# Kernel tuning notes

Measured on AMD Instinct MI355X. Metric: run time of the kernel, lower is better.

The kernel has to match this reference:

```python
import jax, jax.numpy as jnp
from jax import lax
import numpy as np

# Lorentz manifold parameter (geoopt convention: hyperboloid <x,x>_L = -K, x0 = sqrt(K + ||x_s||^2)).
# curvature=1.0, learn_curvature=False in the selected config.
K = 1.0
SK = 1.0  # sqrt(K)
EPS = 1e-5


def l_inner(u, v):
    # Minkowski inner product with keepdim: -u0*v0 + <u_space, v_space>
    uv = u * v
    return -uv[..., :1] + jnp.sum(uv[..., 1:], axis=-1, keepdims=True)


def add_time(space):
    # CustomLorentz.add_time / calc_time: recompute time component from space part
    t = jnp.sqrt(jnp.sum(space * space, axis=-1, keepdims=True) + K)
    return jnp.concatenate([t, space], axis=-1)


def centroid(x):
    # Lorentz centroid over axis=-2 (CustomLorentz.centroid)
    avg = jnp.mean(x, axis=-2)
    den = jnp.sqrt(jnp.clip(jnp.abs(-l_inner(avg, avg)), 1e-8))
    return SK * avg / den


def lorentz_bn(x, beta, gamma):
    # LorentzBatchNorm (training mode, batch statistics). x: (B, N, C)
    mean = centroid(centroid(x))  # (C,) double centroid for 3D input
    # logmap(mean, x)
    xy = l_inner(mean, x)  # (B,N,1)
    dist = SK * jnp.arccosh(jnp.clip(-xy / K, 1.0 + 1e-7))
    nomin = x + (xy / K) * mean
    den = jnp.sqrt(jnp.clip(l_inner(nomin, nomin), 1e-8))
    u = dist * nomin / den
    # transp0back(mean, u): parallel transport mean -> origin
    o = jnp.zeros_like(mean).at[0].set(SK)
    u = u + (-SK * u[..., :1]) / (K + SK * mean[0]) * (mean + o)
    # Frechet variance (mean tangent norm) and rescale
    var = jnp.mean(jnp.linalg.norm(u, axis=-1))
    u = u * (gamma / (var + EPS))
    # transp0(beta, u): origin -> beta, then expmap at beta
    ob = jnp.zeros_like(beta).at[0].set(SK)
    u = u + l_inner(beta, u) / (K + SK * beta[0]) * (ob + beta)
    nu = jnp.sqrt(jnp.clip(l_inner(u, u), 1e-8))
    return jnp.cosh(nu / SK) * beta + SK * jnp.sinh(nu / SK) * u / nu


def lorentz_conv_block(x, W, b, beta, gamma):
    # LConv2d_Block: LorentzConv2d(3x3, stride 2, pad 1) + LorentzBatchNorm2d + relu-on-space
    B = x.shape[0]
    KK = 9  # kernel_size**2
    p = lax.conv_general_dilated_patches(
        jnp.transpose(x, (0, 3, 1, 2)), (3, 3), (2, 2), ((1, 1), (1, 1)))
    p = jnp.transpose(p, (0, 2, 3, 1))  # (B,Ho,Wo,C*9), channel-major = torch.nn.Unfold layout
    # Lorentz direct concatenation of the 9 patch points: fix zero padding, rescale time
    t = jnp.maximum(p[..., :KK], SK)
    t_new = jnp.sqrt(jnp.sum(t * t, axis=-1, keepdims=True) - (KK - 1) * K)
    pre = jnp.concatenate([t_new, p[..., KK:]], axis=-1)
    # LorentzFullyConnected: linear, drop produced time column, recompute time
    lin = jnp.einsum('bhwi,oi->bhwo', pre, W) + b
    y = add_time(lin[..., 1:])
    Ho, Wo, C = y.shape[1], y.shape[2], y.shape[3]
    y = lorentz_bn(y.reshape(B, Ho * Wo, C), beta, gamma).reshape(B, Ho, Wo, C)
    return add_time(jax.nn.relu(y[..., 1:]))


def setup_inputs() -> dict:
    key = jax.random.key(0)
    ks = jax.random.split(key, 12)
    B = 32
    inp = {"x": jax.random.normal(ks[0], (B, 3, 256, 256), jnp.float32)}
    # (out_channels, (in_channels-1)*9+1) per LorentzConv2d linearized kernel
    dims = [(33, 28), (65, 289), (129, 577), (257, 1153)]
    for i, (o, ii) in enumerate(dims):
        inp[f"conv_w{i}"] = 0.02 * jax.random.normal(ks[1 + i], (o, ii), jnp.float32)
        inp[f"conv_b{i}"] = jnp.zeros((o,), jnp.float32)
        inp[f"bn_beta{i}"] = jnp.zeros((o,), jnp.float32).at[0].set(SK)  # manifold origin
        inp[f"bn_gamma{i}"] = jnp.ones((1,), jnp.float32)
    flat = 16 * 16 * 256  # z_h*z_w*z_filters
    inp["wm"] = 0.02 * jax.random.normal(ks[8], (513, flat + 1), jnp.float32)
    inp["bm"] = jnp.zeros((513,), jnp.float32)
    inp["wv"] = 0.02 * jax.random.normal(ks[9], (513, flat + 1), jnp.float32)
    inp["bv"] = jnp.zeros((513,), jnp.float32)
    return inp


def reference(x, conv_w0, conv_b0, bn_beta0, bn_gamma0,
              conv_w1, conv_b1, bn_beta1, bn_gamma1,
              conv_w2, conv_b2, bn_beta2, bn_gamma2,
              conv_w3, conv_b3, bn_beta3, bn_gamma3,
              wm, bm, wv, bv):
    h = jnp.transpose(x, (0, 2, 3, 1))  # (B,H,W,3)
    # F.pad with zero time then manifold.projx == recompute time from space
    h = add_time(h)
    for W, b, beta, g in ((conv_w0, conv_b0, bn_beta0, bn_gamma0),
                          (conv_w1, conv_b1, bn_beta1, bn_gamma1),
                          (conv_w2, conv_b2, bn_beta2, bn_gamma2),
                          (conv_w3, conv_b3, bn_beta3, bn_gamma3)):
        h = lorentz_conv_block(h, W, b, beta, g)
    # lorentz_flatten: concat space parts, recompute single time
    h = add_time(h[..., 1:].reshape(h.shape[0], -1))  # (B, 65537)
    mean = add_time((h @ wm.T + bm)[..., 1:])          # (B, 513)
    varl = add_time((h @ wv.T + bv)[..., 1:])
    var = jnp.maximum(jax.nn.softplus(varl[..., 1:]), EPS)  # (B, 512)
    return mean, var
```

## Files before the change

kernel.cpp:

```cpp
#include <hip/hip_runtime.h>
#include <math.h>

#define DEV __device__ __forceinline__

typedef float f32x4 __attribute__((ext_vector_type(4)));
typedef __bf16 bf16x8 __attribute__((ext_vector_type(8)));

DEV unsigned short f2bf(float f){
  unsigned int u = __float_as_uint(f);
  u = (u + 0x7FFFu + ((u >> 16) & 1u)) >> 16;
  return (unsigned short)u;
}
DEV float bf2f(unsigned short s){
  return __uint_as_float(((unsigned int)s) << 16);
}

DEV float wredf(float v){
  v += __shfl_xor(v, 32, 64);
  v += __shfl_xor(v, 16, 64);
  v += __shfl_xor(v, 8, 64);
  v += __shfl_xor(v, 4, 64);
  v += __shfl_xor(v, 2, 64);
  v += __shfl_xor(v, 1, 64);
  return v;
}

__global__ void h0_kernel(const float* __restrict__ x, unsigned short* __restrict__ h0){
  int idx = blockIdx.x*256 + threadIdx.x;
  int b = idx >> 16, p = idx & 65535;
  const float* xb = x + (size_t)b*3*65536;
  float v0 = xb[p], v1 = xb[65536 + p], v2 = xb[131072 + p];
  float t = sqrtf(v0*v0 + v1*v1 + v2*v2 + 1.f);
  ushort4 o;
  o.x = f2bf(t); o.y = f2bf(v0); o.z = f2bf(v1); o.w = f2bf(v2);
  *(ushort4*)&h0[(size_t)idx*4] = o;
}

__global__ void wrepack_kernel(const float* __restrict__ w, unsigned short* __restrict__ dst,
                               int coutm1, int cs, int K, int krow){
  int idx = blockIdx.x*256 + threadIdx.x;
  if (idx >= coutm1*krow) return;
  int n = idx / krow, kk = idx - n*krow;
  unsigned short v = 0;
  if (kk < 9*cs){
    int kp = kk / cs, c = kk - kp*cs;
    v = f2bf(w[(size_t)(n+1)*K + 1 + c*9 + kp]);
  }
  dst[idx] = v;
}

__global__ __launch_bounds__(256) void conv0_mfma_kernel(
    const unsigned short* __restrict__ h0bf, const unsigned short* __restrict__ wrp0,
    const float* __restrict__ Wm, const float* __restrict__ bias,
    float* __restrict__ y, float* __restrict__ red){
  __shared__ __align__(16) unsigned short A_lds[64][40];
  __shared__ __align__(16) unsigned short B_lds[32][40];
  __shared__ float Tsq[64][9];
  __shared__ float tA[64];
  __shared__ float bins[33];
  int tid = threadIdx.x;
  int tile = blockIdx.x, b = blockIdx.y;
  int oy0 = (tile >> 4) * 8, ox0 = (tile & 15) * 8;
  for (int i = tid; i < 320; i += 256){
    uint4 z = {0,0,0,0};
    *(uint4*)&A_lds[i/5][(i%5)*8] = z;
  }
  if (tid < 128)
    *(uint4*)&B_lds[tid>>2][(tid&3)*8] = *(const uint4*)&wrp0[(size_t)(tid>>2)*32 + (tid&3)*8];
  if (tid < 33) bins[tid] = 0.f;
  __syncthreads();
  for (int i = tid; i < 576; i += 256){
    int m = i/9, kp = i - (i/9)*9;
    int py = oy0 + (m >> 3), px = ox0 + (m & 7);
    int iy = py*2 + kp/3 - 1, ix = px*2 + kp%3 - 1;
    ushort4 v = {0x3F80, 0, 0, 0};
    if ((unsigned)iy < 256u && (unsigned)ix < 256u)
      v = *(const ushort4*)&h0bf[((size_t)(b*256 + iy)*256 + ix)*4];
    A_lds[m][kp*3 + 0] = v.y;
    A_lds[m][kp*3 + 1] = v.z;
    A_lds[m][kp*3 + 2] = v.w;
    float tv = fmaxf(bf2f(v.x), 1.f);
    Tsq[m][kp] = tv*tv;
  }
  __syncthreads();
  if (tid < 64){
    float s = 0.f;
    #pragma unroll
    for (int kp = 0; kp < 9; ++kp) s += Tsq[tid][kp];
    tA[tid] = sqrtf(fmaxf(s - 8.f, 0.f));
  }
  int wave = tid >> 6, lane = tid & 63;
  int row = lane & 15, kb = lane >> 4;
  int m0 = wave * 16;
  f32x4 zero = {0.f,0.f,0.f,0.f};
  f32x4 acc0 = zero, acc1 = zero;
  bf16x8 af = *(const bf16x8*)&A_lds[m0 + row][kb*8];
  bf16x8 b0 = *(const bf16x8*)&B_lds[row][kb*8];
  bf16x8 b1 = *(const bf16x8*)&B_lds[16 + row][kb*8];
  acc0 = __builtin_amdgcn_mfma_f32_16x16x32_bf16(af, b0, acc0, 0, 0, 0);
  acc1 = __builtin_amdgcn_mfma_f32_16x16x32_bf16(af, b1, acc1, 0, 0, 0);
  __syncthreads();
  int o0 = row + 1, o1 = 17 + row;
  float bv0 = bias[o0], w00 = Wm[(size_t)o0*28];
  float bv1 = bias[o1], w01 = Wm[(size_t)o1*28];
  float v0[4], v1[4];
  #pragma unroll
  for (int r = 0; r < 4; ++r){
    int m = m0 + kb*4 + r;
    v0[r] = acc0[r] + bv0 + tA[m]*w00;
    v1[r] = acc1[r] + bv1 + tA[m]*w01;
    int py = oy0 + (m >> 3), px = ox0 + (m & 7);
    size_t pb_ = ((size_t)(b*128 + py)*128 + px)*33;
    y[pb_ + o0] = v0[r];
    y[pb_ + o1] = v1[r];
  }
  float sq[4];
  #pragma unroll
  for (int r = 0; r < 4; ++r) sq[r] = v0[r]*v0[r] + v1[r]*v1[r];
  #pragma unroll
  for (int msk = 1; msk <= 8; msk <<= 1)
    #pragma unroll
    for (int r = 0; r < 4; ++r) sq[r] += __shfl_xor(sq[r], msk, 64);
  float tvs = 0.f;
  #pragma unroll
  for (int r = 0; r < 4; ++r){
    float tv = sqrtf(sq[r] + 1.f);
    tvs += tv;
    if (row == 0){
      int m = m0 + kb*4 + r;
      int py = oy0 + (m >> 3), px = ox0 + (m & 7);
      y[((size_t)(b*128 + py)*128 + px)*33] = tv;
    }
  }
  float cs0 = v0[0] + v0[1] + v0[2] + v0[3];
  float cs1 = v1[0] + v1[1] + v1[2] + v1[3];
  cs0 += __shfl_xor(cs0, 16, 64); cs0 += __shfl_xor(cs0, 32, 64);
  cs1 += __shfl_xor(cs1, 16, 64); cs1 += __shfl_xor(cs1, 32, 64);
  tvs += __shfl_xor(tvs, 16, 64); tvs += __shfl_xor(tvs, 32, 64);
  if (kb == 0){
    atomicAdd(&bins[o0], cs0);
    atomicAdd(&bins[o1], cs1);
    if (row == 0) atomicAdd(&bins[0], tvs);
  }
  __syncthreads();
  if (tid < 33) atomicAdd(&red[(size_t)b*33 + tid], bins[tid]);
}

template<int CS, int COUT, int KPC, int NSPLIT, bool FUSE>
__global__ __launch_bounds__(256) void conv2_mfma_kernel(
    const unsigned short* __restrict__ sp_in, const unsigned short* __restrict__ t_in,
    const unsigned short* __restrict__ wrp, const float* __restrict__ Wm,
    const float* __restrict__ bias, float* __restrict__ y,
    float* __restrict__ red, int Hin, int Ho){
  constexpr int KROW = 9*CS;
  __shared__ __align__(16) unsigned short A_lds[64][40];
  __shared__ __align__(16) unsigned short B_lds[64][40];
  __shared__ float tA[64];
  __shared__ float ssqS[FUSE ? 64 : 1];
  __shared__ float binsS[FUSE ? COUT : 1];
  int tid = threadIdx.x;
  int wave = tid >> 6, lane = tid & 63;
  int tilesX = Ho >> 3;
  int tile = blockIdx.x, b = blockIdx.y;
  int zt = blockIdx.z / NSPLIT, sp = blockIdx.z % NSPLIT;
  int zbase = zt * 64;
  int oy0 = (tile / tilesX) * 8, ox0 = (tile % tilesX) * 8;
  int m0 = (wave >> 1) * 32, n0 = (wave & 1) * 32;
  int row = lane & 15, kb = lane >> 4;
  if (FUSE){
    if (tid < 64) ssqS[tid] = 0.f;
    for (int i = tid; i < COUT; i += 256) binsS[i] = 0.f;
  }
  if (sp == 0 && tid < 64){
    int m = tid;
    int py = oy0 + (m >> 3), px = ox0 + (m & 7);
    float s = 0.f;
    #pragma unroll
    for (int kp = 0; kp < 9; ++kp){
      int iy = py*2 + kp/3 - 1, ix = px*2 + kp%3 - 1;
      float tv = 1.f;
      if ((unsigned)iy < (unsigned)Hin && (unsigned)ix < (unsigned)Hin)
        tv = fmaxf(bf2f(t_in[(size_t)(b*Hin + iy)*Hin + ix]), 1.f);
      s = fmaf(tv, tv, s);
    }
    tA[m] = sqrtf(fmaxf(s - 8.f, 0.f));
  }
  f32x4 zero = {0.f,0.f,0.f,0.f};
  f32x4 acc[2][2] = {{zero,zero},{zero,zero}};
  int ar = tid >> 2, aseg = tid & 3;
  int apy = oy0 + (ar >> 3), apx = ox0 + (ar & 7);
  for (int ch = sp*KPC; ch < sp*KPC + KPC; ++ch){
    int kglob = ch * 32;
    int kp = kglob / CS, c0 = kglob % CS;
    int iy = apy*2 + kp/3 - 1, ix = apx*2 + kp%3 - 1;
    uint4 va = {0,0,0,0};
    if ((unsigned)iy < (unsigned)Hin && (unsigned)ix < (unsigned)Hin)
      va = *(const uint4*)&sp_in[((size_t)(b*Hin + iy)*Hin + ix)*CS + c0 + aseg*8];
    uint4 vb = *(const uint4*)&wrp[(size_t)(zbase + ar)*KROW + kglob + aseg*8];
    __syncthreads();
    *(uint4*)&A_lds[ar][aseg*8] = va;
    *(uint4*)&B_lds[ar][aseg*8] = vb;
    __syncthreads();
    bf16x8 af0 = *(const bf16x8*)&A_lds[m0 + row][kb*8];
    bf16x8 af1 = *(const bf16x8*)&A_lds[m0 + 16 + row][kb*8];
    bf16x8 bf0 = *(const bf16x8*)&B_lds[n0 + row][kb*8];
    bf16x8 bf1 = *(const bf16x8*)&B_lds[n0 + 16 + row][kb*8];
    acc[0][0] = __builtin_amdgcn_mfma_f32_16x16x32_bf16(af0, bf0, acc[0][0], 0, 0, 0);
    acc[0][1] = __builtin_amdgcn_mfma_f32_16x16x32_bf16(af0, bf1, acc[0][1], 0, 0, 0);
    acc[1][0] = __builtin_amdgcn_mfma_f32_16x16x32_bf16(af1, bf0, acc[1][0], 0, 0, 0);
    acc[1][1] = __builtin_amdgcn_mfma_f32_16x16x32_bf16(af1, bf1, acc[1][1], 0, 0, 0);
  }
  __syncthreads();
  float vv[2][2][4];
  #pragma unroll
  for (int mi = 0; mi < 2; ++mi)
    #pragma unroll
    for (int ni = 0; ni < 2; ++ni){
      int col = n0 + 16*ni + row;
      int o = zbase + 1 + col;
      float bv = 0.f, w0 = 0.f;
      if (sp == 0){ bv = bias[o]; w0 = Wm[(size_t)o*(KROW + 1)]; }
      #pragma unroll
      for (int r = 0; r < 4; ++r){
        int m = m0 + 16*mi + kb*4 + r;
        int py = oy0 + (m >> 3), px = ox0 + (m & 7);
        size_t idx = ((size_t)(b*Ho + py)*Ho + px)*COUT + o;
        float val = acc[mi][ni][r];
        if (sp == 0) val += bv + tA[m]*w0;
        vv[mi][ni][r] = val;
        if (NSPLIT > 1) atomicAdd(&y[idx], val);
        else            y[idx] = val;
      }
    }
  if (FUSE){
    float sq[2][4];
    #pragma unroll
    for (int mi = 0; mi < 2; ++mi)
      #pragma unroll
      for (int r = 0; r < 4; ++r)
        sq[mi][r] = vv[mi][0][r]*vv[mi][0][r] + vv[mi][1][r]*vv[mi][1][r];
    #pragma unroll
    for (int msk = 1; msk <= 8; msk <<= 1)
      #pragma unroll
      for (int mi = 0; mi < 2; ++mi)
        #pragma unroll
        for (int r = 0; r < 4; ++r) sq[mi][r] += __shfl_xor(sq[mi][r], msk, 64);
    if (row == 0){
      #pragma unroll
      for (int mi = 0; mi < 2; ++mi)
        #pragma unroll
        for (int r = 0; r < 4; ++r)
          atomicAdd(&ssqS[m0 + 16*mi + kb*4 + r], sq[mi][r]);
    }
    float cs[2];
    #pragma unroll
    for (int ni = 0; ni < 2; ++ni){
      cs[ni] = 0.f;
      #pragma unroll
      for (int mi = 0; mi < 2; ++mi)
        #pragma unroll
        for (int r = 0; r < 4; ++r) cs[ni] += vv[mi][ni][r];
      cs[ni] += __shfl_xor(cs[ni], 16, 64);
      cs[ni] += __shfl_xor(cs[ni], 32, 64);
    }
    if (kb == 0){
      atomicAdd(&binsS[1 + n0 + row], cs[0]);
      atomicAdd(&binsS[1 + n0 + 16 + row], cs[1]);
    }
    __syncthreads();
    if (tid < 64){
      float tv = sqrtf(ssqS[tid] + 1.f);
      int py = oy0 + (tid >> 3), px = ox0 + (tid & 7);
      y[((size_t)(b*Ho + py)*Ho + px)*COUT] = tv;
      atomicAdd(&binsS[0], tv);
    }
    __syncthreads();
    for (int i = tid; i < COUT; i += 256)
      atomicAdd(&red[(size_t)b*COUT + i], binsS[i]);
  }
}

template<int C, int TP>
__global__ __launch_bounds__(256) void time_tile_kernel(float* __restrict__ y){
  constexpr int TPR = 256 / TP;
  __shared__ float tile[TP*C];
  int tid = threadIdx.x;
  size_t base = (size_t)blockIdx.x * TP * C;
  for (int i = tid; i < TP*C; i += 256) tile[i] = y[base + i];
  __syncthreads();
  int r = tid / TPR, seg = tid % TPR;
  float ss = 0.f;
  for (int c = 1 + seg; c < C; c += TPR){ float v = tile[r*C + c]; ss = fmaf(v, v, ss); }
  #pragma unroll
  for (int m = TPR/2; m >= 1; m >>= 1) ss += __shfl_xor(ss, m, 64);
  if (seg == 0) y[base + (size_t)r*C] = sqrtf(ss + 1.f);
}

template<int C>
__global__ __launch_bounds__(256) void rsum_coal_kernel(const float* __restrict__ y,
    float* __restrict__ red, int N, int BPB){
  constexpr int S = (4096 / C) * C;
  __shared__ float bins[C];
  int tid = threadIdx.x;
  for (int i = tid; i < C; i += 256) bins[i] = 0.f;
  int b = blockIdx.y, blk = blockIdx.x;
  size_t per = (size_t)(N / BPB) * C;
  const float* yb = y + (size_t)b*N*C + (size_t)blk*per;
  float a[16];
  #pragma unroll
  for (int k = 0; k < 16; ++k) a[k] = 0.f;
  for (size_t off = 0; off < per; off += S){
    #pragma unroll
    for (int k = 0; k < 16; ++k){
      int e = k*256 + tid;
      if (e < S && off + e < per) a[k] += yb[off + e];
    }
  }
  __syncthreads();
  #pragma unroll
  for (int k = 0; k < 16; ++k){
    int e = k*256 + tid;
    if (e < S) atomicAdd(&bins[e % C], a[k]);
  }
  __syncthreads();
  for (int i = tid; i < C; i += 256) atomicAdd(&red[(size_t)b*C + i], bins[i]);
}

__global__ void cent1_kernel(float* __restrict__ red, float* __restrict__ cent1,
                             int N, int C){
  __shared__ float s[256];
  int b = blockIdx.x, tid = threadIdx.x;
  float va = 0.f, vb = 0.f;
  if (tid < C){ va = red[(size_t)b*C + tid]; red[(size_t)b*C + tid] = 0.f; }
  if (tid + 256 < C){ vb = red[(size_t)b*C + tid + 256]; red[(size_t)b*C + tid + 256] = 0.f; }
  va /= (float)N; vb /= (float)N;
  float pr = ((tid == 0) ? -va*va : va*va) + vb*vb;
  s[tid] = pr; __syncthreads();
  for (int st = 128; st; st >>= 1){ if (tid < st) s[tid] += s[tid+st]; __syncthreads(); }
  float den = sqrtf(fmaxf(fabsf(s[0]), 1e-8f));
  if (tid < C) cent1[(size_t)b*C + tid] = va / den;
  if (tid + 256 < C) cent1[(size_t)b*C + tid + 256] = vb / den;
}

__global__ void stats2_kernel(const float* __restrict__ cent1, float* __restrict__ mean,
                              float* __restrict__ scal, int C){
  __shared__ float s[256];
  int tid = threadIdx.x;
  float a0=0.f,a1=0.f,a2=0.f,a3=0.f, c0=0.f,c1=0.f,c2=0.f,c3=0.f;
  #pragma unroll
  for (int b = 0; b < 32; b += 4){
    const float* r0 = cent1 + (size_t)b*C;
    const float* r1 = r0 + C;
    const float* r2 = r0 + 2*(size_t)C;
    const float* r3 = r0 + 3*(size_t)C;
    if (tid < C){ a0 += r0[tid]; a1 += r1[tid]; a2 += r2[tid]; a3 += r3[tid]; }
    if (tid + 256 < C){
      c0 += r0[tid+256]; c1 += r1[tid+256]; c2 += r2[tid+256]; c3 += r3[tid+256];
    }
  }
  float va = ((a0+a1)+(a2+a3)) * 0.03125f;
  float vb = ((c0+c1)+(c2+c3)) * 0.03125f;
  float pr = ((tid == 0) ? -va*va : va*va) + vb*vb;
  s[tid] = pr; __syncthreads();
  for (int st = 128; st; st >>= 1){ if (tid < st) s[tid] += s[tid+st]; __syncthreads(); }
  float den2 = sqrtf(fmaxf(fabsf(s[0]), 1e-8f));
  if (tid < C) mean[tid] = va / den2;
  if (tid + 256 < C) mean[tid + 256] = vb / den2;
  if (tid < 40) scal[tid] = 0.f;
}

template<int C>
__global__ __launch_bounds__(256) void bn_var_t_kernel(const float* __restrict__ y,
    const float* __restrict__ mean, float* __restrict__ scal, int P){
  __shared__ float sm[C];
  __shared__ float part[4];
  for (int i = threadIdx.x; i < C; i += 256) sm[i] = mean[i];
  __syncthreads();
  float acc = 0.f;
  int stride = gridDim.x * 256;
  for (int p = blockIdx.x*256 + threadIdx.x; p < P; p += stride){
    const float* yp = y + (size_t)p * C;
    float a[C];
    float d1 = 0.f;
    #pragma unroll
    for (int c = 0; c < C; ++c){
      a[c] = yp[c];
      float pr = a[c]*sm[c];
      d1 += (c == 0) ? -pr : pr;
    }
    float xy = d1;
    float dist = acoshf(fmaxf(-xy, 1.f + 1e-7f));
    float d2 = 0.f;
    #pragma unroll
    for (int c = 0; c < C; ++c){
      a[c] = fmaf(xy, sm[c], a[c]);
      float pr = a[c]*a[c];
      d2 += (c == 0) ? -pr : pr;
    }
    float den = sqrtf(fmaxf(d2, 1e-8f));
    float sc = dist / den;
    float corr = -(a[0]*sc) / (1.f + sm[0]);
    float ns = 0.f;
    #pragma unroll
    for (int c = 0; c < C; ++c){
      float uc = fmaf(corr, sm[c] + ((c == 0) ? 1.f : 0.f), a[c]*sc);
      ns = fmaf(uc, uc, ns);
    }
    acc += sqrtf(ns);
  }
  acc = wredf(acc);
  if ((threadIdx.x & 63) == 0) part[threadIdx.x >> 6] = acc;
  __syncthreads();
  if (threadIdx.x == 0)
    atomicAdd(scal, part[0] + part[1] + part[2] + part[3]);
}

template<int C>
__global__ __launch_bounds__(256) void bn_apply_sp_kernel(const float* __restrict__ y,
    const float* __restrict__ mean, const float* __restrict__ beta,
    const float* __restrict__ gamma, const float* __restrict__ scal,
    unsigned short* __restrict__ sp_out, unsigned short* __restrict__ t_out, int P){
  __shared__ float sm[C];
  __shared__ float sb[C];
  for (int i = threadIdx.x; i < C; i += 256){ sm[i] = mean[i]; sb[i] = beta[i]; }
  __syncthreads();
  int p = blockIdx.x*256 + threadIdx.x;
  if (p >= P) return;
  const float* yp = y + (size_t)p * C;
  float a[C];
  float d1 = 0.f;
  #pragma unroll
  for (int c = 0; c < C; ++c){
    a[c] = yp[c];
    float pr = a[c]*sm[c];
    d1 += (c == 0) ? -pr : pr;
  }
  float xy = d1;
  float dist = acoshf(fmaxf(-xy, 1.f + 1e-7f));
  float d2 = 0.f;
  #pragma unroll
  for (int c = 0; c < C; ++c){
    a[c] = fmaf(xy, sm[c], a[c]);
    float pr = a[c]*a[c];
    d2 += (c == 0) ? -pr : pr;
  }
  float den = sqrtf(fmaxf(d2, 1e-8f));
  float sc = dist / den;
  float corr = -(a[0]*sc) / (1.f + sm[0]);
  float var = scal[0] / (float)P;
  float g = gamma[0] / (var + 1e-5f);
  #pragma unroll
  for (int c = 0; c < C; ++c)
    a[c] = fmaf(corr, sm[c] + ((c == 0) ? 1.f : 0.f), a[c]*sc) * g;
  float d3 = 0.f;
  #pragma unroll
  for (int c = 0; c < C; ++c){
    float pr = a[c]*sb[c];
    d3 += (c == 0) ? -pr : pr;
  }
  float cb = d3 / (1.f + sb[0]);
  float d4 = 0.f;
  #pragma unroll
  for (int c = 0; c < C; ++c){
    a[c] = fmaf(cb, sb[c] + ((c == 0) ? 1.f : 0.f), a[c]);
    float pr = a[c]*a[c];
    d4 += (c == 0) ? -pr : pr;
  }
  float nu = sqrtf(fmaxf(d4, 1e-8f));
  float ch = coshf(nu), shn = sinhf(nu) / nu;
  unsigned short* hp = sp_out + (size_t)p * (C - 1);
  float ssum = 0.f;
  #pragma unroll
  for (int c = 1; c < C; ++c){
    float r = fmaxf(fmaf(ch, sb[c], shn*a[c]), 0.f);
    hp[c-1] = f2bf(r);
    ssum = fmaf(r, r, ssum);
  }
  t_out[p] = f2bf(sqrtf(ssum + 1.f));
}

__global__ void bn_var_kernel(const float* __restrict__ y, const float* __restrict__ mean,
                              float* __restrict__ scal, int P, int C){
  __shared__ float smean[260];
  __shared__ float part[4];
  for (int i = threadIdx.x; i < C; i += blockDim.x) smean[i] = mean[i];
  __syncthreads();
  int wv = threadIdx.x >> 6, lane = threadIdx.x & 63;
  int nwaves = gridDim.x * 4;
  float m0 = smean[0];
  float ms[5];
  #pragma unroll
  for (int j = 0; j < 5; ++j){
    int c = lane + 64*j;
    ms[j] = (c < C) ? smean[c] : 0.f;
  }
  float vsum = 0.f;
  for (int p = blockIdx.x*4 + wv; p < P; p += nwaves){
    const float* yp = y + (size_t)p * C;
    float yv[5], nom[5];
    #pragma unroll
    for (int j = 0; j < 5; ++j){
      int c = lane + 64*j;
      yv[j] = (c < C) ? yp[c] : 0.f;
    }
    float d1 = 0.f;
    #pragma unroll
    for (int j = 0; j < 5; ++j){
      int c = lane + 64*j;
      float prd = yv[j]*ms[j];
      d1 += (c == 0) ? -prd : prd;
    }
    float xy = wredf(d1);
    float dist = acoshf(fmaxf(-xy, 1.f + 1e-7f));
    float d2 = 0.f;
    #pragma unroll
    for (int j = 0; j < 5; ++j){
      int c = lane + 64*j;
      nom[j] = yv[j] + xy*ms[j];
      float prd = nom[j]*nom[j];
      d2 += (c == 0) ? -prd : prd;
    }
    float den = sqrtf(fmaxf(wredf(d2), 1e-8f));
    float sc = dist / den;
    float u0 = __shfl(nom[0], 0, 64) * sc;
    float corr = -u0 / (1.f + m0);
    float nsum = 0.f;
    #pragma unroll
    for (int j = 0; j < 5; ++j){
      int c = lane + 64*j;
      float uc = nom[j]*sc + corr*(ms[j] + ((c == 0) ? 1.f : 0.f));
      nsum += uc*uc;
    }
    nsum = wredf(nsum);
    vsum += sqrtf(nsum);
  }
  if (lane == 0) part[wv] = vsum;
  __syncthreads();
  if (threadIdx.x == 0)
    atomicAdd(scal, part[0] + part[1] + part[2] + part[3]);
}

__global__ void bn_apply_flat_kernel(const float* __restrict__ y, const float* __restrict__ mean,
                                     const float* __restrict__ beta, const float* __restrict__ gamma,
                                     const float* __restrict__ scal_in, float* __restrict__ scal,
                                     float* __restrict__ flat, int P, int C){
  __shared__ float smean[260];
  __shared__ float sbeta[260];
  for (int i = threadIdx.x; i < C; i += blockDim.x){ smean[i] = mean[i]; sbeta[i] = beta[i]; }
  __syncthreads();
  int wv = threadIdx.x >> 6, lane = threadIdx.x & 63;
  int p = blockIdx.x*4 + wv;
  if (p >= P) return;
  const float* yp = y + (size_t)p * C;
  float yv[5], ms[5], bs[5], nom[5], uc[5], u2[5];
  #pragma unroll
  for (int j = 0; j < 5; ++j){
    int c = lane + 64*j;
    yv[j] = (c < C) ? yp[c] : 0.f;
    ms[j] = (c < C) ? smean[c] : 0.f;
    bs[j] = (c < C) ? sbeta[c] : 0.f;
  }
  float m0 = smean[0], b0 = sbeta[0];
  float d1 = 0.f;
  #pragma unroll
  for (int j = 0; j < 5; ++j){
    int c = lane + 64*j;
    float prd = yv[j]*ms[j];
    d1 += (c == 0) ? -prd : prd;
  }
  float xy = wredf(d1);
  float dist = acoshf(fmaxf(-xy, 1.f + 1e-7f));
  float d2 = 0.f;
  #pragma unroll
  for (int j = 0; j < 5; ++j){
    nom[j] = yv[j] + xy*ms[j];
    int c = lane + 64*j;
    float prd = nom[j]*nom[j];
    d2 += (c == 0) ? -prd : prd;
  }
  float den = sqrtf(fmaxf(wredf(d2), 1e-8f));
  float sc = dist / den;
  float u0 = __shfl(nom[0], 0, 64) * sc;
  float corr = -u0 / (1.f + m0);
  float var = scal_in[0] / (float)P;
  float g = gamma[0] / (var + 1e-5f);
  #pragma unroll
  for (int j = 0; j < 5; ++j){
    int c = lane + 64*j;
    uc[j] = (nom[j]*sc + corr*(ms[j] + ((c == 0) ? 1.f : 0.f))) * g;
  }
  float d3 = 0.f;
  #pragma unroll
  for (int j = 0; j < 5; ++j){
    int c = lane + 64*j;
    float prd = uc[j]*bs[j];
    d3 += (c == 0) ? -prd : prd;
  }
  float cb = wredf(d3) / (1.f + b0);
  float d4 = 0.f;
  #pragma unroll
  for (int j = 0; j < 5; ++j){
    int c = lane + 64*j;
    u2[j] = uc[j] + cb*(bs[j] + ((c == 0) ? 1.f : 0.f));
    float prd = u2[j]*u2[j];
    d4 += (c == 0) ? -prd : prd;
  }
  float nu = sqrtf(fmaxf(wredf(d4), 1e-8f));
  float ch = coshf(nu), shn = sinhf(nu) / nu;
  float ssum = 0.f;
  int b = p >> 8, n = p & 255;
  float* hp = flat + (size_t)b*65537 + 1 + (size_t)n*256;
  #pragma unroll
  for (int j = 0; j < 5; ++j){
    int c = lane + 64*j;
    if (c > 0 && c < C){
      float r = ch*sbeta[c] + shn*u2[j];
      r = fmaxf(r, 0.f);
      hp[c-1] = r;
      ssum += r*r;
    }
  }
  ssum = wredf(ssum);
  if (lane == 0) atomicAdd(&scal[1 + b], ssum);
}

__global__ void flat_time_kernel(float* __restrict__ flat, const float* __restrict__ scal){
  int b = threadIdx.x;
  if (b < 32) flat[(size_t)b*65537] = sqrtf(scal[1 + b] + 1.f);
}

__global__ void wtail_kernel(const float* __restrict__ wm, const float* __restrict__ wv,
                             float* __restrict__ wtail){
  int i = blockIdx.x*256 + threadIdx.x;
  if (i >= 1024) return;
  wtail[i] = (i < 512) ? wm[(size_t)(i + 1)*65537 + 65536]
                       : wv[(size_t)(i - 511)*65537 + 65536];
}

__global__ __launch_bounds__(256) void fgemm_mfma_kernel(const float* __restrict__ wm,
    const float* __restrict__ wv, const float* __restrict__ flat,
    float* __restrict__ mvacc){
  __shared__ __align__(16) unsigned short A_lds[64][136];
  __shared__ __align__(16) unsigned short B_lds[32][136];
  int tid = threadIdx.x;
  int wave = tid >> 6, lane = tid & 63;
  int kc = blockIdx.x * 512;
  int ob = blockIdx.y * 64;
  int row = lane & 15, kb = lane >> 4;
  int rA0 = tid >> 3, sA0 = tid & 7;
  int rA1 = rA0 + 32;
  int o0 = ob + rA0, o1 = ob + rA1;
  const float* pA0 = ((o0 < 512) ? wm + (size_t)(o0 + 1)*65537
                                 : wv + (size_t)(o0 - 511)*65537) + kc + sA0*16;
  const float* pA1 = ((o1 < 512) ? wm + (size_t)(o1 + 1)*65537
                                 : wv + (size_t)(o1 - 511)*65537) + kc + sA0*16;
  const float* pB = flat + (size_t)rA0*65537 + kc + sA0*16;

  float ra0[16], ra1[16], rb[16];
  #pragma unroll
  for (int j = 0; j < 16; ++j){ ra0[j] = pA0[j]; ra1[j] = pA1[j]; rb[j] = pB[j]; }

  f32x4 zero = {0.f, 0.f, 0.f, 0.f};
  f32x4 acc[2] = {zero, zero};
  for (int sc = 0; sc < 4; ++sc){
    union { unsigned short u[16]; uint4 q[2]; } k0, k1, k2;
    #pragma unroll
    for (int j = 0; j < 16; ++j){ k0.u[j] = f2bf(ra0[j]); k1.u[j] = f2bf(ra1[j]); k2.u[j] = f2bf(rb[j]); }
    *(uint4*)&A_lds[rA0][sA0*16]     = k0.q[0];
    *(uint4*)&A_lds[rA0][sA0*16 + 8] = k0.q[1];
    *(uint4*)&A_lds[rA1][sA0*16]     = k1.q[0];
    *(uint4*)&A_lds[rA1][sA0*16 + 8] = k1.q[1];
    *(uint4*)&B_lds[rA0][sA0*16]     = k2.q[0];
    *(uint4*)&B_lds[rA0][sA0*16 + 8] = k2.q[1];
    __syncthreads();
    if (sc < 3){
      int off = (sc + 1)*128;
      #pragma unroll
      for (int j = 0; j < 16; ++j){ ra0[j] = pA0[off + j]; ra1[j] = pA1[off + j]; rb[j] = pB[off + j]; }
    }
    int m0 = wave*16;
    #pragma unroll
    for (int ks = 0; ks < 4; ++ks){
      bf16x8 af = *(const bf16x8*)&A_lds[m0 + row][ks*32 + kb*8];
      bf16x8 b0 = *(const bf16x8*)&B_lds[row][ks*32 + kb*8];
      bf16x8 b1 = *(const bf16x8*)&B_lds[16 + row][ks*32 + kb*8];
      acc[0] = __builtin_amdgcn_mfma_f32_16x16x32_bf16(af, b0, acc[0], 0, 0, 0);
      acc[1] = __builtin_amdgcn_mfma_f32_16x16x32_bf16(af, b1, acc[1], 0, 0, 0);
    }
    __syncthreads();
  }
  int m0 = wave*16;
  #pragma unroll
  for (int nf = 0; nf < 2; ++nf){
    int b = nf*16 + row;
    #pragma unroll
    for (int r = 0; r < 4; ++r){
      int m = m0 + kb*4 + r;
      atomicAdd(&mvacc[(size_t)(ob + m)*32 + b], acc[nf][r]);
    }
  }
}

__global__ void finalize_kernel(const float* __restrict__ mvacc, const float* __restrict__ bm,
                                const float* __restrict__ bv,
                                const float* __restrict__ wtail,
                                const float* __restrict__ flat, float* __restrict__ out){
  __shared__ float s[256];
  int b = blockIdx.x, tid = threadIdx.x;
  float hl = flat[(size_t)b*65537 + 65536];
  float m0 = mvacc[tid*32 + b] + bm[tid + 1] + wtail[tid] * hl;
  float m1 = mvacc[(tid + 256)*32 + b] + bm[tid + 257] + wtail[tid + 256] * hl;
  s[tid] = m0*m0 + m1*m1; __syncthreads();
  for (int st = 128; st; st >>= 1){ if (tid < st) s[tid] += s[tid+st]; __syncthreads(); }
  float t = sqrtf(s[0] + 1.f);
  float* om = out + (size_t)b*513;
  om[1 + tid] = m0;
  om[1 + tid + 256] = m1;
  if (tid == 0) om[0] = t;
  float v0 = mvacc[(512 + tid)*32 + b] + bv[tid + 1] + wtail[512 + tid] * hl;
  float v1 = mvacc[(512 + tid + 256)*32 + b] + bv[tid + 257] + wtail[768 + tid] * hl;
  float sp0 = fmaxf(v0, 0.f) + log1pf(expf(-fabsf(v0)));
  float sp1 = fmaxf(v1, 0.f) + log1pf(expf(-fabsf(v1)));
  float* ov = out + 32*513 + (size_t)b*512;
  ov[tid] = fmaxf(sp0, 1e-5f);
  ov[tid + 256] = fmaxf(sp1, 1e-5f);
}

extern "C" void kernel_launch(void* const* d_in, const int* in_sizes, int n_in,
                              void* d_out, int out_size, void* d_ws, size_t ws_size,
                              hipStream_t stream){
  const float* x  = (const float*)d_in[0];
  const float* cw[4] = {(const float*)d_in[1], (const float*)d_in[5], (const float*)d_in[9],  (const float*)d_in[13]};
  const float* cb[4] = {(const float*)d_in[2], (const float*)d_in[6], (const float*)d_in[10], (const float*)d_in[14]};
  const float* bb[4] = {(const float*)d_in[3], (const float*)d_in[7], (const float*)d_in[11], (const float*)d_in[15]};
  const float* bg[4] = {(const float*)d_in[4], (const float*)d_in[8], (const float*)d_in[12], (const float*)d_in[16]};
  const float* wm = (const float*)d_in[17];
  const float* bm = (const float*)d_in[18];
  const float* wv = (const float*)d_in[19];
  const float* bv = (const float*)d_in[20];
  float* ws = (float*)d_ws;

  float* Y = ws;
  unsigned short* h0bf = (unsigned short*)(ws + 17500000);
  unsigned short* Sp   = (unsigned short*)(ws + 22000000);
  unsigned short* Tc   = (unsigned short*)(ws + 30500000);
  float* flatp = ws + 36500000;
  float* red   = ws + 40500000;
  float* cent1 = ws + 40600000;
  float* meanp = ws + 40610000;
  float* scal  = ws + 40611000;
  float* mvacc = ws + 40620000;
  float* wtail = ws + 40660000;
  unsigned short* cwb0 = (unsigned short*)(ws + 40700000);
  unsigned short* cwb1 = (unsigned short*)(ws + 40710000);
  unsigned short* cwb2 = (unsigned short*)(ws + 40730000);
  unsigned short* cwb3 = (unsigned short*)(ws + 40780000);

  wrepack_kernel<<<4, 256, 0, stream>>>(cw[0], cwb0, 32, 3, 28, 32);
  wrepack_kernel<<<72, 256, 0, stream>>>(cw[1], cwb1, 64, 32, 289, 288);
  wrepack_kernel<<<288, 256, 0, stream>>>(cw[2], cwb2, 128, 64, 577, 576);
  wrepack_kernel<<<1152, 256, 0, stream>>>(cw[3], cwb3, 256, 128, 1153, 1152);
  wtail_kernel<<<4, 256, 0, stream>>>(wm, wv, wtail);
  hipMemsetAsync(mvacc, 0, 32768*sizeof(float), stream);
  hipMemsetAsync(red, 0, 32*257*sizeof(float), stream);

  h0_kernel<<<8192, 256, 0, stream>>>(x, h0bf);

  const int HoA[4]   = {128, 64, 32, 16};
  const int CoutA[4] = {33, 65, 129, 257};
  const int BPBA[4]  = {64, 32, 16, 8};

  for (int i = 0; i < 4; ++i){
    int Ho = HoA[i], Cout = CoutA[i], BPB = BPBA[i];
    int N = Ho * Ho;
    int P = 32 * N;
    switch (i){
      case 0:
        conv0_mfma_kernel<<<dim3(256,32), 256, 0, stream>>>(h0bf, cwb0, cw[0], cb[0], Y, red);
        break;
      case 1:
        conv2_mfma_kernel<32,65,9,1,true><<<dim3(64,32,1), 256, 0, stream>>>(Sp, Tc, cwb1, cw[1], cb[1], Y, red, 128, 64);
        break;
      case 2:
        hipMemsetAsync(Y, 0, (size_t)P*Cout*sizeof(float), stream);
        conv2_mfma_kernel<64,129,9,2,false><<<dim3(16,32,4), 256, 0, stream>>>(Sp, Tc, cwb2, cw[2], cb[2], Y, red, 64, 32);
        break;
      case 3:
        hipMemsetAsync(Y, 0, (size_t)P*Cout*sizeof(float), stream);
        conv2_mfma_kernel<128,257,9,4,false><<<dim3(4,32,16), 256, 0, stream>>>(Sp, Tc, cwb3, cw[3], cb[3], Y, red, 32, 16);
        break;
    }
    if (i >= 2){
      switch (i){
        case 2:
          time_tile_kernel<129,64><<<P/64, 256, 0, stream>>>(Y);
          rsum_coal_kernel<129><<<dim3(BPB,32), 256, 0, stream>>>(Y, red, N, BPB);
          break;
        case 3:
          time_tile_kernel<257,32><<<P/32, 256, 0, stream>>>(Y);
          rsum_coal_kernel<257><<<dim3(BPB,32), 256, 0, stream>>>(Y, red, N, BPB);
          break;
      }
    }
    cent1_kernel<<<32, 256, 0, stream>>>(red, cent1, N, Cout);
    stats2_kernel<<<1, 256, 0, stream>>>(cent1, meanp, scal, Cout);
    int pb = P / 256;
    int vb = min(pb, 2048);
    switch (i){
      case 0:
        bn_var_t_kernel<33><<<vb, 256, 0, stream>>>(Y, meanp, scal, P);
        bn_apply_sp_kernel<33><<<pb, 256, 0, stream>>>(Y, meanp, bb[i], bg[i], scal, Sp, Tc, P);
        break;
      case 1:
        bn_var_t_kernel<65><<<vb, 256, 0, stream>>>(Y, meanp, scal, P);
        bn_apply_sp_kernel<65><<<pb, 256, 0, stream>>>(Y, meanp, bb[i], bg[i], scal, Sp, Tc, P);
        break;
      case 2:
        bn_var_t_kernel<129><<<vb, 256, 0, stream>>>(Y, meanp, scal, P);
        bn_apply_sp_kernel<129><<<pb, 256, 0, stream>>>(Y, meanp, bb[i], bg[i], scal, Sp, Tc, P);
        break;
      case 3:
        bn_var_kernel<<<min((P + 3)/4, 2048), 256, 0, stream>>>(Y, meanp, scal, P, Cout);
        bn_apply_flat_kernel<<<(P + 3)/4, 256, 0, stream>>>(Y, meanp, bb[i], bg[i], scal, scal, flatp, P, Cout);
        break;
    }
  }

  flat_time_kernel<<<1, 64, 0, stream>>>(flatp, scal);
  fgemm_mfma_kernel<<<dim3(128, 16), 256, 0, stream>>>(wm, wv, flatp, mvacc);
  finalize_kernel<<<32, 256, 0, stream>>>(mvacc, bm, bv, wtail, flatp, (float*)d_out);
}
```

Measured before the change: 587.7 us.

## Store early conv outputs in bf16 and merge setup and stats kernels

Layers 0 and 1 now write their conv output Y as bf16 instead of fp32, and the batch-norm variance and apply kernels read it back as bf16, which halves the traffic on the largest intermediate tensors. The weight repacks, tail copy and two memsets are merged into one setup kernel, and the two centroid kernels become a single one-block stats kernel, cutting launch count. The cost is extra rounding of pre-norm activations, which may hurt accuracy. A leftover unused helper function is also added.

```diff
diff --git a/kernel.cpp b/kernel.cpp
--- a/kernel.cpp
+++ b/kernel.cpp
@@ -36,23 +36,71 @@
   *(ushort4*)&h0[(size_t)idx*4] = o;
 }
 
-__global__ void wrepack_kernel(const float* __restrict__ w, unsigned short* __restrict__ dst,
-                               int coutm1, int cs, int K, int krow){
-  int idx = blockIdx.x*256 + threadIdx.x;
-  if (idx >= coutm1*krow) return;
-  int n = idx / krow, kk = idx - n*krow;
+DEV void repack_one(const float* w, unsigned short* dst, int kk, int n,
+                    int cs, int K){
   unsigned short v = 0;
   if (kk < 9*cs){
     int kp = kk / cs, c = kk - kp*cs;
     v = f2bf(w[(size_t)(n+1)*K + 1 + c*9 + kp]);
   }
-  dst[idx] = v;
+  dst[(size_t)n*((9*cs + 31)/32*32 >= 9*cs ? 0 : 0)] = v;
+}
+
+__global__ void setup_kernel(const float* __restrict__ cw0, const float* __restrict__ cw1,
+                             const float* __restrict__ cw2, const float* __restrict__ cw3,
+                             const float* __restrict__ wm, const float* __restrict__ wv,
+                             unsigned short* __restrict__ cwb0, unsigned short* __restrict__ cwb1,
+                             unsigned short* __restrict__ cwb2, unsigned short* __restrict__ cwb3,
+                             float* __restrict__ wtail, float* __restrict__ mvacc,
+                             float* __restrict__ red){
+  int idx = blockIdx.x*256 + threadIdx.x;
+  if (idx < 1024){
+    int n = idx >> 5, kk = idx & 31;
+    unsigned short v = 0;
+    if (kk < 27){ int kp = kk/3, c = kk - kp*3; v = f2bf(cw0[(size_t)(n+1)*28 + 1 + c*9 + kp]); }
+    cwb0[idx] = v;
+    return;
+  }
+  idx -= 1024;
+  if (idx < 18432){
+    int n = idx / 288, kk = idx - n*288;
+    cwb1[idx] = f2bf(cw1[(size_t)(n+1)*289 + 1 + (kk>>5)*9 + ((kk & 31) == kk - (kk>>5)*32 ? 0 : 0) + 0]);
+    {
+      int kp = kk / 32, c = kk - kp*32;
+      cwb1[idx] = f2bf(cw1[(size_t)(n+1)*289 + 1 + c*9 + kp]);
+    }
+    return;
+  }
+  idx -= 18432;
+  if (idx < 73728){
+    int n = idx / 576, kk = idx - n*576;
+    int kp = kk / 64, c = kk - kp*64;
+    cwb2[idx] = f2bf(cw2[(size_t)(n+1)*577 + 1 + c*9 + kp]);
+    return;
+  }
+  idx -= 73728;
+  if (idx < 294912){
+    int n = idx / 1152, kk = idx - n*1152;
+    int kp = kk / 128, c = kk - kp*128;
+    cwb3[idx] = f2bf(cw3[(size_t)(n+1)*1153 + 1 + c*9 + kp]);
+    return;
+  }
+  idx -= 294912;
+  if (idx < 1024){
+    wtail[idx] = (idx < 512) ? wm[(size_t)(idx + 1)*65537 + 65536]
+                             : wv[(size_t)(idx - 511)*65537 + 65536];
+    return;
+  }
+  idx -= 1024;
+  if (idx < 32768){ mvacc[idx] = 0.f; return; }
+  idx -= 32768;
+  if (idx < 8224) red[idx] = 0.f;
 }
 
 __global__ __launch_bounds__(256) void conv0_mfma_kernel(
     const unsigned short* __restrict__ h0bf, const unsigned short* __restrict__ wrp0,
     const float* __restrict__ Wm, const float* __restrict__ bias,
-    float* __restrict__ y, float* __restrict__ red){
+    unsigned short* __restrict__ y, float* __restrict__ red){
   __shared__ __align__(16) unsigned short A_lds[64][40];
   __shared__ __align__(16) unsigned short B_lds[32][40];
   __shared__ float Tsq[64][9];
@@ -111,8 +159,8 @@
     v1[r] = acc1[r] + bv1 + tA[m]*w01;
     int py = oy0 + (m >> 3), px = ox0 + (m & 7);
     size_t pb_ = ((size_t)(b*128 + py)*128 + px)*33;
-    y[pb_ + o0] = v0[r];
-    y[pb_ + o1] = v1[r];
+    y[pb_ + o0] = f2bf(v0[r]);
+    y[pb_ + o1] = f2bf(v1[r]);
   }
   float sq[4];
   #pragma unroll
@@ -129,7 +177,7 @@
     if (row == 0){
       int m = m0 + kb*4 + r;
       int py = oy0 + (m >> 3), px = ox0 + (m & 7);
-      y[((size_t)(b*128 + py)*128 + px)*33] = tv;
+      y[((size_t)(b*128 + py)*128 + px)*33] = f2bf(tv);
     }
   }
   float cs0 = v0[0] + v0[1] + v0[2] + v0[3];
@@ -146,11 +194,11 @@
   if (tid < 33) atomicAdd(&red[(size_t)b*33 + tid], bins[tid]);
 }
 
-template<int CS, int COUT, int KPC, int NSPLIT, bool FUSE>
+template<int CS, int COUT, int KPC, int NSPLIT, bool FUSE, bool YBF>
 __global__ __launch_bounds__(256) void conv2_mfma_kernel(
     const unsigned short* __restrict__ sp_in, const unsigned short* __restrict__ t_in,
     const unsigned short* __restrict__ wrp, const float* __restrict__ Wm,
-    const float* __restrict__ bias, float* __restrict__ y,
+    const float* __restrict__ bias, void* __restrict__ yv_,
     float* __restrict__ red, int Hin, int Ho){
   constexpr int KROW = 9*CS;
   __shared__ __align__(16) unsigned short A_lds[64][40];
@@ -158,6 +206,8 @@
   __shared__ float tA[64];
   __shared__ float ssqS[FUSE ? 64 : 1];
   __shared__ float binsS[FUSE ? COUT : 1];
+  float* yf = (float*)yv_;
+  unsigned short* yh = (unsigned short*)yv_;
   int tid = threadIdx.x;
   int wave = tid >> 6, lane = tid & 63;
   int tilesX = Ho >> 3;
@@ -228,8 +278,9 @@
         float val = acc[mi][ni][r];
         if (sp == 0) val += bv + tA[m]*w0;
         vv[mi][ni][r] = val;
-        if (NSPLIT > 1) atomicAdd(&y[idx], val);
-        else            y[idx] = val;
+        if (YBF)              yh[idx] = f2bf(val);
+        else if (NSPLIT > 1)  atomicAdd(&yf[idx], val);
+        else                  yf[idx] = val;
       }
     }
   if (FUSE){
@@ -271,7 +322,9 @@
     if (tid < 64){
       float tv = sqrtf(ssqS[tid] + 1.f);
       int py = oy0 + (tid >> 3), px = ox0 + (tid & 7);
-      y[((size_t)(b*Ho + py)*Ho + px)*COUT] = tv;
+      size_t idx = ((size_t)(b*Ho + py)*Ho + px)*COUT;
+      if (YBF) yh[idx] = f2bf(tv);
+      else     yf[idx] = tv;
       atomicAdd(&binsS[0], tv);
     }
     __syncthreads();
@@ -326,40 +379,43 @@
   for (int i = tid; i < C; i += 256) atomicAdd(&red[(size_t)b*C + i], bins[i]);
 }
 
-__global__ void cent1_kernel(float* __restrict__ red, float* __restrict__ cent1,
-                             int N, int C){
-  __shared__ float s[256];
-  int b = blockIdx.x, tid = threadIdx.x;
-  float va = 0.f, vb = 0.f;
-  if (tid < C){ va = red[(size_t)b*C + tid]; red[(size_t)b*C + tid] = 0.f; }
-  if (tid + 256 < C){ vb = red[(size_t)b*C + tid + 256]; red[(size_t)b*C + tid + 256] = 0.f; }
-  va /= (float)N; vb /= (float)N;
-  float pr = ((tid == 0) ? -va*va : va*va) + vb*vb;
-  s[tid] = pr; __syncthreads();
-  for (int st = 128; st; st >>= 1){ if (tid < st) s[tid] += s[tid+st]; __syncthreads(); }
-  float den = sqrtf(fmaxf(fabsf(s[0]), 1e-8f));
-  if (tid < C) cent1[(size_t)b*C + tid] = va / den;
-  if (tid + 256 < C) cent1[(size_t)b*C + tid + 256] = vb / den;
-}
-
-__global__ void stats2_kernel(const float* __restrict__ cent1, float* __restrict__ mean,
-                              float* __restrict__ scal, int C){
+__global__ __launch_bounds__(256) void stats_kernel(float* __restrict__ red,
+    float* __restrict__ mean, float* __restrict__ scal, int N, int C){
+  __shared__ float cent[8224];
   __shared__ float s[256];
   int tid = threadIdx.x;
-  float a0=0.f,a1=0.f,a2=0.f,a3=0.f, c0=0.f,c1=0.f,c2=0.f,c3=0.f;
-  #pragma unroll
-  for (int b = 0; b < 32; b += 4){
-    const float* r0 = cent1 + (size_t)b*C;
-    const float* r1 = r0 + C;
-    const float* r2 = r0 + 2*(size_t)C;
-    const float* r3 = r0 + 3*(size_t)C;
-    if (tid < C){ a0 += r0[tid]; a1 += r1[tid]; a2 += r2[tid]; a3 += r3[tid]; }
-    if (tid + 256 < C){
-      c0 += r0[tid+256]; c1 += r1[tid+256]; c2 += r2[tid+256]; c3 += r3[tid+256];
-    }
-  }
-  float va = ((a0+a1)+(a2+a3)) * 0.03125f;
-  float vb = ((c0+c1)+(c2+c3)) * 0.03125f;
+  int wave = tid >> 6, lane = tid & 63;
+  for (int j = 0; j < 8; ++j){
+    int b = wave*8 + j;
+    float va[5]; float d = 0.f;
+    #pragma unroll
+    for (int k = 0; k < 5; ++k){
+      int c = lane + 64*k;
+      float v = 0.f;
+      if (c < C){ v = red[(size_t)b*C + c] / (float)N; red[(size_t)b*C + c] = 0.f; }
+      va[k] = v;
+      float pr = v*v;
+      d += (c == 0) ? -pr : pr;
+    }
+    float den = sqrtf(fmaxf(fabsf(wredf(d)), 1e-8f));
+    #pragma unroll
+    for (int k = 0; k < 5; ++k){
+      int c = lane + 64*k;
+      if (c < C) cent[b*C + c] = va[k] / den;
+    }
+  }
+  __syncthreads();
+  float va = 0.f, vb = 0.f;
+  if (tid < C){
+    #pragma unroll 4
+    for (int b = 0; b < 32; ++b) va += cent[b*C + tid];
+    va *= 0.03125f;
+  }
+  if (tid + 256 < C){
+    #pragma unroll 4
+    for (int b = 0; b < 32; ++b) vb += cent[b*C + tid + 256];
+    vb *= 0.03125f;
+  }
   float pr = ((tid == 0) ? -va*va : va*va) + vb*vb;
   s[tid] = pr; __syncthreads();
   for (int st = 128; st; st >>= 1){ if (tid < st) s[tid] += s[tid+st]; __syncthreads(); }
@@ -369,22 +425,23 @@
   if (tid < 40) scal[tid] = 0.f;
 }
 
-template<int C>
-__global__ __launch_bounds__(256) void bn_var_t_kernel(const float* __restrict__ y,
+template<int C, bool YBF>
+__global__ __launch_bounds__(256) void bn_var_t_kernel(const void* __restrict__ yv_,
     const float* __restrict__ mean, float* __restrict__ scal, int P){
   __shared__ float sm[C];
   __shared__ float part[4];
+  const float* yf = (const float*)yv_;
+  const unsigned short* yh = (const unsigned short*)yv_;
   for (int i = threadIdx.x; i < C; i += 256) sm[i] = mean[i];
   __syncthreads();
   float acc = 0.f;
   int stride = gridDim.x * 256;
   for (int p = blockIdx.x*256 + threadIdx.x; p < P; p += stride){
-    const float* yp = y + (size_t)p * C;
     float a[C];
     float d1 = 0.f;
     #pragma unroll
     for (int c = 0; c < C; ++c){
-      a[c] = yp[c];
+      a[c] = YBF ? bf2f(yh[(size_t)p*C + c]) : yf[(size_t)p*C + c];
       float pr = a[c]*sm[c];
       d1 += (c == 0) ? -pr : pr;
     }
@@ -415,23 +472,24 @@
     atomicAdd(scal, part[0] + part[1] + part[2] + part[3]);
 }
 
-template<int C>
-__global__ __launch_bounds__(256) void bn_apply_sp_kernel(const float* __restrict__ y,
+template<int C, bool YBF>
+__global__ __launch_bounds__(256) void bn_apply_sp_kernel(const void* __restrict__ yv_,
     const float* __restrict__ mean, const float* __restrict__ beta,
     const float* __restrict__ gamma, const float* __restrict__ scal,
     unsigned short* __restrict__ sp_out, unsigned short* __restrict__ t_out, int P){
   __shared__ float sm[C];
   __shared__ float sb[C];
+  const float* yf = (const float*)yv_;
+  const unsigned short* yh = (const unsigned short*)yv_;
   for (int i = threadIdx.x; i < C; i += 256){ sm[i] = mean[i]; sb[i] = beta[i]; }
   __syncthreads();
   int p = blockIdx.x*256 + threadIdx.x;
   if (p >= P) return;
-  const float* yp = y + (size_t)p * C;
   float a[C];
   float d1 = 0.f;
   #pragma unroll
   for (int c = 0; c < C; ++c){
-    a[c] = yp[c];
+    a[c] = YBF ? bf2f(yh[(size_t)p*C + c]) : yf[(size_t)p*C + c];
     float pr = a[c]*sm[c];
     d1 += (c == 0) ? -pr : pr;
   }
@@ -497,17 +555,17 @@
   float vsum = 0.f;
   for (int p = blockIdx.x*4 + wv; p < P; p += nwaves){
     const float* yp = y + (size_t)p * C;
-    float yv[5], nom[5];
+    float yvv[5], nom[5];
     #pragma unroll
     for (int j = 0; j < 5; ++j){
       int c = lane + 64*j;
-      yv[j] = (c < C) ? yp[c] : 0.f;
+      yvv[j] = (c < C) ? yp[c] : 0.f;
     }
     float d1 = 0.f;
     #pragma unroll
     for (int j = 0; j < 5; ++j){
       int c = lane + 64*j;
-      float prd = yv[j]*ms[j];
+      float prd = yvv[j]*ms[j];
       d1 += (c == 0) ? -prd : prd;
     }
     float xy = wredf(d1);
@@ -516,7 +574,7 @@
     #pragma unroll
     for (int j = 0; j < 5; ++j){
       int c = lane + 64*j;
-      nom[j] = yv[j] + xy*ms[j];
+      nom[j] = yvv[j] + xy*ms[j];
       float prd = nom[j]*nom[j];
       d2 += (c == 0) ? -prd : prd;
     }
@@ -552,11 +610,11 @@
   int p = blockIdx.x*4 + wv;
   if (p >= P) return;
   const float* yp = y + (size_t)p * C;
-  float yv[5], ms[5], bs[5], nom[5], uc[5], u2[5];
+  float yvv[5], ms[5], bs[5], nom[5], uc[5], u2[5];
   #pragma unroll
   for (int j = 0; j < 5; ++j){
     int c = lane + 64*j;
-    yv[j] = (c < C) ? yp[c] : 0.f;
+    yvv[j] = (c < C) ? yp[c] : 0.f;
     ms[j] = (c < C) ? smean[c] : 0.f;
     bs[j] = (c < C) ? sbeta[c] : 0.f;
   }
@@ -565,7 +623,7 @@
   #pragma unroll
   for (int j = 0; j < 5; ++j){
     int c = lane + 64*j;
-    float prd = yv[j]*ms[j];
+    float prd = yvv[j]*ms[j];
     d1 += (c == 0) ? -prd : prd;
   }
   float xy = wredf(d1);
@@ -573,7 +631,7 @@
   float d2 = 0.f;
   #pragma unroll
   for (int j = 0; j < 5; ++j){
-    nom[j] = yv[j] + xy*ms[j];
+    nom[j] = yvv[j] + xy*ms[j];
     int c = lane + 64*j;
     float prd = nom[j]*nom[j];
     d2 += (c == 0) ? -prd : prd;
@@ -627,14 +685,6 @@
 __global__ void flat_time_kernel(float* __restrict__ flat, const float* __restrict__ scal){
   int b = threadIdx.x;
   if (b < 32) flat[(size_t)b*65537] = sqrtf(scal[1 + b] + 1.f);
-}
-
-__global__ void wtail_kernel(const float* __restrict__ wm, const float* __restrict__ wv,
-                             float* __restrict__ wtail){
-  int i = blockIdx.x*256 + threadIdx.x;
-  if (i >= 1024) return;
-  wtail[i] = (i < 512) ? wm[(size_t)(i + 1)*65537 + 65536]
-                       : wv[(size_t)(i - 511)*65537 + 65536];
 }
 
 __global__ __launch_bounds__(256) void fgemm_mfma_kernel(const float* __restrict__ wm,
@@ -741,12 +791,12 @@
   float* ws = (float*)d_ws;
 
   float* Y = ws;
+  unsigned short* Yh = (unsigned short*)ws;
   unsigned short* h0bf = (unsigned short*)(ws + 17500000);
   unsigned short* Sp   = (unsigned short*)(ws + 22000000);
   unsigned short* Tc   = (unsigned short*)(ws + 30500000);
   float* flatp = ws + 36500000;
   float* red   = ws + 40500000;
-  float* cent1 = ws + 40600000;
   float* meanp = ws + 40610000;
   float* scal  = ws + 40611000;
   float* mvacc = ws + 40620000;
@@ -756,13 +806,8 @@
   unsigned short* cwb2 = (unsigned short*)(ws + 40730000);
   unsigned short* cwb3 = (unsigned short*)(ws + 40780000);
 
-  wrepack_kernel<<<4, 256, 0, stream>>>(cw[0], cwb0, 32, 3, 28, 32);
-  wrepack_kernel<<<72, 256, 0, stream>>>(cw[1], cwb1, 64, 32, 289, 288);
-  wrepack_kernel<<<288, 256, 0, stream>>>(cw[2], cwb2, 128, 64, 577, 576);
-  wrepack_kernel<<<1152, 256, 0, stream>>>(cw[3], cwb3, 256, 128, 1153, 1152);
-  wtail_kernel<<<4, 256, 0, stream>>>(wm, wv, wtail);
-  hipMemsetAsync(mvacc, 0, 32768*sizeof(float), stream);
-  hipMemsetAsync(red, 0, 32*257*sizeof(float), stream);
+  setup_kernel<<<1681, 256, 0, stream>>>(cw[0], cw[1], cw[2], cw[3], wm, wv,
+                                         cwb0, cwb1, cwb2, cwb3, wtail, mvacc, red);
 
   h0_kernel<<<8192, 256, 0, stream>>>(x, h0bf);
 
@@ -776,18 +821,18 @@
     int P = 32 * N;
     switch (i){
       case 0:
-        conv0_mfma_kernel<<<dim3(256,32), 256, 0, stream>>>(h0bf, cwb0, cw[0], cb[0], Y, red);
+        conv0_mfma_kernel<<<dim3(256,32), 256, 0, stream>>>(h0bf, cwb0, cw[0], cb[0], Yh, red);
         break;
       case 1:
-        conv2_mfma_kernel<32,65,9,1,true><<<dim3(64,32,1), 256, 0, stream>>>(Sp, Tc, cwb1, cw[1], cb[1], Y, red, 128, 64);
+        conv2_mfma_kernel<32,65,9,1,true,true><<<dim3(64,32,1), 256, 0, stream>>>(Sp, Tc, cwb1, cw[1], cb[1], (void*)Yh, red, 128, 64);
         break;
       case 2:
         hipMemsetAsync(Y, 0, (size_t)P*Cout*sizeof(float), stream);
-        conv2_mfma_kernel<64,129,9,2,false><<<dim3(16,32,4), 256, 0, stream>>>(Sp, Tc, cwb2, cw[2], cb[2], Y, red, 64, 32);
+        conv2_mfma_kernel<64,129,9,2,false,false><<<dim3(16,32,4), 256, 0, stream>>>(Sp, Tc, cwb2, cw[2], cb[2], (void*)Y, red, 64, 32);
         break;
       case 3:
         hipMemsetAsync(Y, 0, (size_t)P*Cout*sizeof(float), stream);
-        conv2_mfma_kernel<128,257,9,4,false><<<dim3(4,32,16), 256, 0, stream>>>(Sp, Tc, cwb3, cw[3], cb[3], Y, red, 32, 16);
+        conv2_mfma_kernel<128,257,9,4,false,false><<<dim3(4,32,16), 256, 0, stream>>>(Sp, Tc, cwb3, cw[3], cb[3], (void*)Y, red, 32, 16);
         break;
     }
     if (i >= 2){
@@ -802,22 +847,21 @@
           break;
       }
     }
-    cent1_kernel<<<32, 256, 0, stream>>>(red, cent1, N, Cout);
-    stats2_kernel<<<1, 256, 0, stream>>>(cent1, meanp, scal, Cout);
+    stats_kernel<<<1, 256, 0, stream>>>(red, meanp, scal, N, Cout);
     int pb = P / 256;
     int vb = min(pb, 2048);
     switch (i){
       case 0:
-        bn_var_t_kernel<33><<<vb, 256, 0, stream>>>(Y, meanp, scal, P);
-        bn_apply_sp_kernel<33><<<pb, 256, 0, stream>>>(Y, meanp, bb[i], bg[i], scal, Sp, Tc, P);
+        bn_var_t_kernel<33,true><<<vb, 256, 0, stream>>>((const void*)Yh, meanp, scal, P);
+        bn_apply_sp_kernel<33,true><<<pb, 256, 0, stream>>>((const void*)Yh, meanp, bb[i], bg[i], scal, Sp, Tc, P);
         break;
       case 1:
-        bn_var_t_kernel<65><<<vb, 256, 0, stream>>>(Y, meanp, scal, P);
-        bn_apply_sp_kernel<65><<<pb, 256, 0, stream>>>(Y, meanp, bb[i], bg[i], scal, Sp, Tc, P);
+        bn_var_t_kernel<65,true><<<vb, 256, 0, stream>>>((const void*)Yh, meanp, scal, P);
+        bn_apply_sp_kernel<65,true><<<pb, 256, 0, stream>>>((const void*)Yh, meanp, bb[i], bg[i], scal, Sp, Tc, P);
         break;
       case 2:
-        bn_var_t_kernel<129><<<vb, 256, 0, stream>>>(Y, meanp, scal, P);
-        bn_apply_sp_kernel<129><<<pb, 256, 0, stream>>>(Y, meanp, bb[i], bg[i], scal, Sp, Tc, P);
+        bn_var_t_kernel<129,false><<<vb, 256, 0, stream>>>((const void*)Y, meanp, scal, P);
+        bn_apply_sp_kernel<129,false><<<pb, 256, 0, stream>>>((const void*)Y, meanp, bb[i], bg[i], scal, Sp, Tc, P);
         break;
       case 3:
         bn_var_kernel<<<min((P + 3)/4, 2048), 256, 0, stream>>>(Y, meanp, scal, P, Cout);
```

Measured after the change: 592.3 us. No clear change (+0.8%).
